# Performance work log

Hardware: AMD Instinct MI355X
Metric: run time of the kernel (lower is better)

## Reference

```python
import jax, jax.numpy as jnp
import numpy as np
import math

NUM_HEADS = 8


def setup_inputs() -> dict:
    key = jax.random.key(0)
    ks = jax.random.split(key, 6)
    b, s, e = 4, 2048, 512
    x = jax.random.normal(ks[0], (b, s, e), dtype=jnp.float32)
    # 0/1 adjacency matrix as float (it multiplies the scores in the module)
    adj = jax.random.randint(ks[1], (b, s, s), 0, 2).astype(jnp.float32)
    scale = 0.02
    Wqkv_w = jax.random.normal(ks[2], (3 * e, e), dtype=jnp.float32) * scale
    Wqkv_b = jax.random.normal(ks[3], (3 * e,), dtype=jnp.float32) * scale
    out_w = jax.random.normal(ks[4], (e, e), dtype=jnp.float32) * scale
    out_b = jax.random.normal(ks[5], (e,), dtype=jnp.float32) * scale
    return {"x": x, "adj": adj, "Wqkv_w": Wqkv_w, "Wqkv_b": Wqkv_b,
            "out_w": out_w, "out_b": out_b}


def reference(x, adj, Wqkv_w, Wqkv_b, out_w, out_b):
    b, s, e = x.shape
    h = NUM_HEADS
    d = e // h
    # fused qkv projection: (b, s, 3*e) -> (b, s, 3, h, d)
    qkv = (x @ Wqkv_w.T + Wqkv_b).reshape(b, s, 3, h, d)
    qkv = jnp.transpose(qkv, (2, 0, 3, 1, 4))  # (3, b, h, s, d)
    q, k, v = qkv[0], qkv[1], qkv[2]
    inv_sqrt_d = 1.0 / math.sqrt(d)
    scores = jnp.einsum('bhqd,bhkd->bhqk', q, k) * inv_sqrt_d
    scores = jnp.clip(scores * adj[:, None, :, :], -10000.0, 10000.0)
    attn = jax.nn.softmax(scores, axis=-1)
    out = jnp.einsum('bhqk,bhkd->bhqd', attn, v)
    out = jnp.transpose(out, (0, 2, 1, 3)).reshape(b, s, e)  # (b, s, h*d)
    return out @ out_w.T + out_b
```

## Files before the change

### kernel.cpp

```cpp
#include <hip/hip_runtime.h>


typedef __attribute__((ext_vector_type(8))) short bf16x8;
typedef __attribute__((ext_vector_type(4))) float f32x4;
typedef __attribute__((ext_vector_type(4))) unsigned short ushort4v;
typedef __attribute__((ext_vector_type(4))) _Float16 f16x4;
typedef __attribute__((ext_vector_type(2))) __fp16 h16x2;

#if __has_builtin(__builtin_amdgcn_exp2f)
#define EXP2F(x) __builtin_amdgcn_exp2f(x)
#else
#define EXP2F(x) exp2f(x)
#endif

#define QSCALE 0.18033688011112042f

__device__ __forceinline__ unsigned short f2bf(float f) {
  unsigned int u = __float_as_uint(f);
  u += 0x7FFFu + ((u >> 16) & 1u);
  return (unsigned short)(u >> 16);
}
__device__ __forceinline__ unsigned short f2h(float f) {
  union { _Float16 h; unsigned short u; } cv;
  cv.h = (_Float16)f;
  return cv.u;
}

__device__ __forceinline__ int sbit(unsigned w, int pos) {
  return ((int)(w << (31 - pos))) >> 31;
}

__device__ __forceinline__ f16x4 pk4(float p0, float p1, float p2, float p3) {
  union { struct { h16x2 a, b; } s; f16x4 v; } u;
  u.s.a = __builtin_amdgcn_cvt_pkrtz(p0, p1);
  u.s.b = __builtin_amdgcn_cvt_pkrtz(p2, p3);
  return u.v;
}

__global__ __launch_bounds__(256) void prep_k(const float* __restrict__ x,
                                              unsigned short* __restrict__ x_bf,
                                              const float* __restrict__ wqkv,
                                              unsigned short* __restrict__ wqkv_bf,
                                              const float* __restrict__ outw,
                                              unsigned short* __restrict__ outw_bf,
                                              const float* __restrict__ adj,
                                              unsigned long long* __restrict__ abits) {
  const int bid = blockIdx.x;
  if (bid < 5120) {
    const float* in; unsigned short* out; int i;
    if (bid < 4096) { in = x; out = x_bf; i = bid * 256 + threadIdx.x; }
    else if (bid < 4864) { in = wqkv; out = wqkv_bf; i = (bid - 4096) * 256 + threadIdx.x; }
    else { in = outw; out = outw_bf; i = (bid - 4864) * 256 + threadIdx.x; }
    float4 v = ((const float4*)in)[i];
    ushort4v o;
    o[0] = f2bf(v.x); o[1] = f2bf(v.y); o[2] = f2bf(v.z); o[3] = f2bf(v.w);
    ((ushort4v*)out)[i] = o;
  } else {
    const int gw = (bid - 5120) * 4 + (threadIdx.x >> 6);
    const int l = threadIdx.x & 63;
    const int b = gw >> 11, q = gw & 2047;
    const float* row = adj + ((size_t)b * 2048 + q) * 2048;
    unsigned long long* ob = abits + (size_t)b * 65536 + q;
#pragma unroll 4
    for (int kt = 0; kt < 32; ++kt) {
      const float v = row[kt * 64 + l];
      const unsigned long long m = __ballot(v != 0.f);
      if (l == 0) ob[(size_t)kt * 2048] = m;
    }
  }
}

template <int MODE>
__global__ __launch_bounds__(256, 3) void gemm128_k(const unsigned short* __restrict__ A,
                                                    const unsigned short* __restrict__ Bt,
                                                    const float* __restrict__ bias, int Kdim,
                                                    int Ntiles, unsigned short* __restrict__ q_out,
                                                    unsigned short* __restrict__ k_out,
                                                    unsigned short* __restrict__ v_out,
                                                    float* __restrict__ f_out) {
  __shared__ union {
    struct { unsigned short A[2][128][40], B[2][128][40]; } s;
    unsigned short T[64][136];
  } u;

  const int t = threadIdx.x;
  const int lane = t & 63, w = t >> 6, ln = lane & 15, quad = lane >> 4;
  const int mt = blockIdx.x / Ntiles, nt = blockIdx.x % Ntiles;
  const int wm = (w >> 1) * 64, wn = (w & 1) * 64;
  const int strow = t >> 2, stcol = (t & 3) * 8;

  const size_t abase = (size_t)(mt * 128 + strow) * Kdim + stcol;
  const size_t bbase = (size_t)(nt * 128 + strow) * Kdim + stcol;

  f32x4 acc[4][4];
#pragma unroll
  for (int i = 0; i < 4; ++i)
#pragma unroll
    for (int j = 0; j < 4; ++j) acc[i][j] = (f32x4){0.f, 0.f, 0.f, 0.f};

  bf16x8 a0 = *(const bf16x8*)(A + abase);
  bf16x8 a1 = *(const bf16x8*)(A + abase + (size_t)64 * Kdim);
  bf16x8 b0 = *(const bf16x8*)(Bt + bbase);
  bf16x8 b1 = *(const bf16x8*)(Bt + bbase + (size_t)64 * Kdim);
  *(bf16x8*)&u.s.A[0][strow][stcol] = a0;
  *(bf16x8*)&u.s.A[0][64 + strow][stcol] = a1;
  *(bf16x8*)&u.s.B[0][strow][stcol] = b0;
  *(bf16x8*)&u.s.B[0][64 + strow][stcol] = b1;
  __syncthreads();

  const int iters = Kdim >> 5;
  for (int it = 0; it < iters; ++it) {
    const int cur = it & 1, nxt = cur ^ 1;

    const int kn = ((it + 1) << 5) & (Kdim - 1);
    a0 = *(const bf16x8*)(A + abase + kn);
    a1 = *(const bf16x8*)(A + abase + (size_t)64 * Kdim + kn);
    b0 = *(const bf16x8*)(Bt + bbase + kn);
    b1 = *(const bf16x8*)(Bt + bbase + (size_t)64 * Kdim + kn);

    bf16x8 bfr[4];
#pragma unroll
    for (int nf = 0; nf < 4; ++nf)
      bfr[nf] = *(const bf16x8*)&u.s.B[cur][wn + nf * 16 + ln][quad * 8];
#pragma unroll
    for (int mf = 0; mf < 4; ++mf) {
      bf16x8 af = *(const bf16x8*)&u.s.A[cur][wm + mf * 16 + ln][quad * 8];
#pragma unroll
      for (int nf = 0; nf < 4; ++nf)
        acc[mf][nf] = __builtin_amdgcn_mfma_f32_16x16x32_bf16(af, bfr[nf], acc[mf][nf], 0, 0, 0);
    }

    if (it + 1 < iters) {
      *(bf16x8*)&u.s.A[nxt][strow][stcol] = a0;
      *(bf16x8*)&u.s.A[nxt][64 + strow][stcol] = a1;
      *(bf16x8*)&u.s.B[nxt][strow][stcol] = b0;
      *(bf16x8*)&u.s.B[nxt][64 + strow][stcol] = b1;
      __syncthreads();
    }
  }

  if (MODE == 0 && nt >= 8) {
    const int bb = mt >> 4, sq0 = (mt & 15) * 128;
#pragma unroll
    for (int half = 0; half < 2; ++half) {
      __syncthreads();
      if ((w & 1) == half) {
#pragma unroll
        for (int nf = 0; nf < 4; ++nf) {
          const float bv = bias[nt * 128 + half * 64 + nf * 16 + ln];
#pragma unroll
          for (int mf = 0; mf < 4; ++mf)
#pragma unroll
            for (int r = 0; r < 4; ++r)
              u.T[nf * 16 + ln][wm + mf * 16 + quad * 4 + r] = f2h(acc[mf][nf][r] + bv);
        }
      }
      __syncthreads();
#pragma unroll
      for (int rep = 0; rep < 4; ++rep) {
        const int row = rep * 16 + (t >> 4), c = t & 15;
        const bf16x8 val = *(const bf16x8*)&u.T[row][c * 8];
        const int hd = (nt - 8) * 128 + half * 64 + row;
        const int hh = hd >> 6, dd = hd & 63;
        *(bf16x8*)(v_out + ((size_t)(bb * 8 + hh) * 64 + dd) * 2048 + sq0 + c * 8) = val;
      }
    }
    return;
  }

#pragma unroll
  for (int mf = 0; mf < 4; ++mf) {
    const int m = mt * 128 + wm + mf * 16 + quad * 4;
#pragma unroll
    for (int nf = 0; nf < 4; ++nf) {
      const int n = nt * 128 + wn + nf * 16 + ln;
      const float bv = bias[n];
      if (MODE == 0) {
        const int hd = n & 511;
        const int hh = hd >> 6, dd = hd & 63;
        const int bb = m >> 11, sq = m & 2047;
        if (n < 512) {
#pragma unroll
          for (int r = 0; r < 4; ++r)
            q_out[((size_t)(bb * 8 + hh) * 2048 + sq + r) * 64 + dd] =
                f2bf((acc[mf][nf][r] + bv) * QSCALE);
        } else {
#pragma unroll
          for (int r = 0; r < 4; ++r)
            k_out[((size_t)(bb * 8 + hh) * 2048 + sq + r) * 64 + dd] = f2bf(acc[mf][nf][r] + bv);
        }
      } else {
#pragma unroll
        for (int r = 0; r < 4; ++r) f_out[(size_t)(m + r) * 512 + n] = acc[mf][nf][r] + bv;
      }
    }
  }
}

__global__ __launch_bounds__(256, 2) void attn_k(const unsigned short* __restrict__ Qg,
                                                 const unsigned short* __restrict__ Kg,
                                                 const unsigned short* __restrict__ Vg,
                                                 const unsigned long long* __restrict__ Mg,
                                                 unsigned short* __restrict__ Og) {
  __shared__ unsigned short K_lds[2][64][72];
  __shared__ unsigned short V_lds[2][64][72];
  __shared__ unsigned long long M_lds[2][128];

  const int t = threadIdx.x;
  const int w = t >> 6, lane = t & 63, ln = lane & 15, quad = lane >> 4;
  const int bh = blockIdx.x & 31, qt = blockIdx.x >> 5, bb = bh >> 3;
  const int sbase = qt * 128;

  const unsigned short* Qp = Qg + (size_t)bh * (2048 * 64);
  const unsigned short* Kp = Kg + (size_t)bh * (2048 * 64);
  const unsigned short* Vp = Vg + (size_t)bh * (64 * 2048);
  const unsigned long long* Mp = Mg + (size_t)bb * 65536 + sbase;

  bf16x8 qf[2][2];
#pragma unroll
  for (int qg = 0; qg < 2; ++qg) {
    const int qrow = sbase + w * 32 + qg * 16 + ln;
    qf[qg][0] = *(const bf16x8*)(Qp + (size_t)qrow * 64 + quad * 8);
    qf[qg][1] = *(const bf16x8*)(Qp + (size_t)qrow * 64 + 32 + quad * 8);
  }

  const _Float16 one_h = (_Float16)((ln == 0) ? 1.0f : 0.0f);
  const f16x4 vf_one = (f16x4){one_h, one_h, one_h, one_h};

  f32x4 acc_o[2][4];
#pragma unroll
  for (int qg = 0; qg < 2; ++qg)
#pragma unroll
    for (int dg = 0; dg < 4; ++dg) acc_o[qg][dg] = (f32x4){0.f, 0.f, 0.f, 0.f};
  f32x4 acc_1[2] = {(f32x4){0.f, 0.f, 0.f, 0.f}, (f32x4){0.f, 0.f, 0.f, 0.f}};

  const int strow = t >> 2;
  const int stcol = (t & 3) * 16;

  const unsigned short* Kl = Kp + (size_t)strow * 64 + stcol;
  const unsigned short* Vl = Vp + (size_t)strow * 2048 + stcol;

  bf16x8 kr0 = *(const bf16x8*)(Kl);
  bf16x8 kr1 = *(const bf16x8*)(Kl + 8);
  bf16x8 vr0 = *(const bf16x8*)(Vl);
  bf16x8 vr1 = *(const bf16x8*)(Vl + 8);
  unsigned long long mreg = (w < 2) ? Mp[w * 64 + lane] : 0ull;
  *(bf16x8*)&K_lds[0][strow][stcol] = kr0;
  *(bf16x8*)&K_lds[0][strow][stcol + 8] = kr1;
  *(bf16x8*)&V_lds[0][strow][stcol] = vr0;
  *(bf16x8*)&V_lds[0][strow][stcol + 8] = vr1;
  if (w < 2) M_lds[0][w * 64 + lane] = mreg;
  __syncthreads();

  const int mq = w * 32 + ln;
  const int qsh = quad * 4;

  for (int kt = 0; kt < 32; ++kt) {
    const int cur = kt & 1, nxt = cur ^ 1;

    kr0 = *(const bf16x8*)(Kl + (size_t)(kt + 1) * 4096);
    kr1 = *(const bf16x8*)(Kl + (size_t)(kt + 1) * 4096 + 8);
    vr0 = *(const bf16x8*)(Vl + (kt + 1) * 64);
    vr1 = *(const bf16x8*)(Vl + (kt + 1) * 64 + 8);
    mreg = (w < 2) ? Mp[(size_t)(kt + 1) * 2048 + w * 64 + lane] : 0ull;

    f32x4 sc[2][4];
#pragma unroll
    for (int nf = 0; nf < 4; ++nf) {
      bf16x8 kf0 = *(const bf16x8*)&K_lds[cur][nf * 16 + ln][quad * 8];
      bf16x8 kf1 = *(const bf16x8*)&K_lds[cur][nf * 16 + ln][32 + quad * 8];
#pragma unroll
      for (int qg = 0; qg < 2; ++qg) {
        f32x4 z = (f32x4){0.f, 0.f, 0.f, 0.f};
        z = __builtin_amdgcn_mfma_f32_16x16x32_bf16(kf0, qf[qg][0], z, 0, 0, 0);
        sc[qg][nf] = __builtin_amdgcn_mfma_f32_16x16x32_bf16(kf1, qf[qg][1], z, 0, 0, 0);
      }
    }

    f16x4 vfa[4][4];
#pragma unroll
    for (int ks = 0; ks < 4; ++ks)
#pragma unroll
      for (int dg = 0; dg < 4; ++dg)
        vfa[ks][dg] = *(const f16x4*)&V_lds[cur][dg * 16 + ln][ks * 16 + quad * 4];

    f16x4 pa[2][4];
#pragma unroll
    for (int qg = 0; qg < 2; ++qg) {
      const unsigned long long m64 = M_lds[cur][mq + qg * 16];
      const unsigned wlo = (unsigned)m64 >> qsh;
      const unsigned whi = (unsigned)(m64 >> 32) >> qsh;
#pragma unroll
      for (int nf = 0; nf < 4; ++nf) {
        const unsigned wm16 = ((nf & 2) ? whi : wlo) >> ((nf & 1) * 16);
        float p[4];
#pragma unroll
        for (int r = 0; r < 4; ++r) {
          const int se = sbit(wm16, r);
          const float s = __int_as_float(__float_as_int(sc[qg][nf][r]) & se);
          p[r] = EXP2F(s);
        }
        pa[qg][nf] = pk4(p[0], p[1], p[2], p[3]);
      }
    }

#pragma unroll
    for (int ks = 0; ks < 4; ++ks)
#pragma unroll
      for (int qg = 0; qg < 2; ++qg) {
#pragma unroll
        for (int dg = 0; dg < 4; ++dg)
          acc_o[qg][dg] =
              __builtin_amdgcn_mfma_f32_16x16x16f16(pa[qg][ks], vfa[ks][dg], acc_o[qg][dg], 0, 0, 0);
        acc_1[qg] = __builtin_amdgcn_mfma_f32_16x16x16f16(pa[qg][ks], vf_one, acc_1[qg], 0, 0, 0);
      }

    if (kt < 31) {
      *(bf16x8*)&K_lds[nxt][strow][stcol] = kr0;
      *(bf16x8*)&K_lds[nxt][strow][stcol + 8] = kr1;
      *(bf16x8*)&V_lds[nxt][strow][stcol] = vr0;
      *(bf16x8*)&V_lds[nxt][strow][stcol + 8] = vr1;
      if (w < 2) M_lds[nxt][w * 64 + lane] = mreg;
      __syncthreads();
    }
  }

  unsigned short* Op = Og + (size_t)bb * 2048 * 512 + (size_t)(bh & 7) * 64;
#pragma unroll
  for (int qg = 0; qg < 2; ++qg)
#pragma unroll
    for (int r = 0; r < 4; ++r) {
      const float inv = 1.0f / __shfl(acc_1[qg][r], quad * 16);
      const int sq = sbase + w * 32 + qg * 16 + quad * 4 + r;
#pragma unroll
      for (int dg = 0; dg < 4; ++dg)
        Op[(size_t)sq * 512 + dg * 16 + ln] = f2bf(acc_o[qg][dg][r] * inv);
    }
}

extern "C" void kernel_launch(void* const* d_in, const int* in_sizes, int n_in, void* d_out,
                              int out_size, void* d_ws, size_t ws_size, hipStream_t stream) {
  const float* x = (const float*)d_in[0];
  const float* adj = (const float*)d_in[1];
  const float* wqkv = (const float*)d_in[2];
  const float* bqkv = (const float*)d_in[3];
  const float* outw = (const float*)d_in[4];
  const float* outb = (const float*)d_in[5];
  float* out = (float*)d_out;

  char* ws = (char*)d_ws;
  unsigned short* x_bf = (unsigned short*)(ws);
  unsigned short* wqkv_bf = (unsigned short*)(ws + 8388608);
  unsigned short* outw_bf = (unsigned short*)(ws + 9961472);
  unsigned long long* abits = (unsigned long long*)(ws + 10485760);
  unsigned short* Qb = (unsigned short*)(ws + 27262976);
  unsigned short* Kb = (unsigned short*)(ws + 35651584);
  unsigned short* Vb = (unsigned short*)(ws + 44040192);
  unsigned short* Ob = (unsigned short*)(ws + 52428800);

  prep_k<<<7168, 256, 0, stream>>>(x, x_bf, wqkv, wqkv_bf, outw, outw_bf, adj, abits);

  gemm128_k<0><<<768, 256, 0, stream>>>(x_bf, wqkv_bf, bqkv, 512, 12, Qb, Kb, Vb, nullptr);

  attn_k<<<512, 256, 0, stream>>>(Qb, Kb, Vb, abits, Ob);

  gemm128_k<1><<<256, 256, 0, stream>>>(Ob, outw_bf, outb, 512, 4, nullptr, nullptr, nullptr, out);
}
```

Measured before the change: 220.1 us.

## Use 16x16x32 f16 MFMA for PV with permuted K rows, XCD-aware GEMM tiling

The attention kernel permutes which K rows each lane loads so the score fragments line up with the K-dimension layout of the wider 16x16x32 f16 MFMA. This halves the number of PV and row-sum MFMA instructions and lets V fragments be read as 8-wide vectors. The K LDS row padding changes from 72 to 76 to move bank conflicts caused by the new access pattern. The GEMM also remaps block indices so that consecutive M tiles are scheduled on the same XCD for better L2 reuse, which adds index arithmetic and relies on the grid size dividing evenly.

```diff
diff --git a/kernel.cpp b/kernel.cpp
--- a/kernel.cpp
+++ b/kernel.cpp
@@ -5,6 +5,7 @@
 typedef __attribute__((ext_vector_type(4))) float f32x4;
 typedef __attribute__((ext_vector_type(4))) unsigned short ushort4v;
 typedef __attribute__((ext_vector_type(4))) _Float16 f16x4;
+typedef __attribute__((ext_vector_type(8))) _Float16 f16x8;
 typedef __attribute__((ext_vector_type(2))) __fp16 h16x2;
 
 #if __has_builtin(__builtin_amdgcn_exp2f)
@@ -30,11 +31,24 @@
   return ((int)(w << (31 - pos))) >> 31;
 }
 
-__device__ __forceinline__ f16x4 pk4(float p0, float p1, float p2, float p3) {
-  union { struct { h16x2 a, b; } s; f16x4 v; } u;
-  u.s.a = __builtin_amdgcn_cvt_pkrtz(p0, p1);
-  u.s.b = __builtin_amdgcn_cvt_pkrtz(p2, p3);
+__device__ __forceinline__ f16x8 pk8(const float* p) {
+  union { struct { h16x2 a, b, c, d; } s; f16x8 v; } u;
+  u.s.a = __builtin_amdgcn_cvt_pkrtz(p[0], p[1]);
+  u.s.b = __builtin_amdgcn_cvt_pkrtz(p[2], p[3]);
+  u.s.c = __builtin_amdgcn_cvt_pkrtz(p[4], p[5]);
+  u.s.d = __builtin_amdgcn_cvt_pkrtz(p[6], p[7]);
   return u.v;
+}
+
+__device__ __forceinline__ f32x4 mfma_pv(f16x8 a, f16x8 b, f32x4 c) {
+#if __has_builtin(__builtin_amdgcn_mfma_f32_16x16x32_f16)
+  return __builtin_amdgcn_mfma_f32_16x16x32_f16(a, b, c, 0, 0, 0);
+#else
+  union { f16x8 v; struct { f16x4 lo, hi; } s; } ua, ub;
+  ua.v = a; ub.v = b;
+  c = __builtin_amdgcn_mfma_f32_16x16x16f16(ua.s.lo, ub.s.lo, c, 0, 0, 0);
+  return __builtin_amdgcn_mfma_f32_16x16x16f16(ua.s.hi, ub.s.hi, c, 0, 0, 0);
+#endif
 }
 
 __global__ __launch_bounds__(256) void prep_k(const float* __restrict__ x,
@@ -85,7 +99,9 @@
 
   const int t = threadIdx.x;
   const int lane = t & 63, w = t >> 6, ln = lane & 15, quad = lane >> 4;
-  const int mt = blockIdx.x / Ntiles, nt = blockIdx.x % Ntiles;
+  const int xcd = blockIdx.x & 7, loc = blockIdx.x >> 3;
+  const int mt = xcd * ((gridDim.x >> 3) / Ntiles) + loc / Ntiles;
+  const int nt = loc % Ntiles;
   const int wm = (w >> 1) * 64, wn = (w & 1) * 64;
   const int strow = t >> 2, stcol = (t & 3) * 8;
 
@@ -202,7 +218,7 @@
                                                  const unsigned short* __restrict__ Vg,
                                                  const unsigned long long* __restrict__ Mg,
                                                  unsigned short* __restrict__ Og) {
-  __shared__ unsigned short K_lds[2][64][72];
+  __shared__ unsigned short K_lds[2][64][76];
   __shared__ unsigned short V_lds[2][64][72];
   __shared__ unsigned long long M_lds[2][128];
 
@@ -225,7 +241,7 @@
   }
 
   const _Float16 one_h = (_Float16)((ln == 0) ? 1.0f : 0.0f);
-  const f16x4 vf_one = (f16x4){one_h, one_h, one_h, one_h};
+  const f16x8 vf_one = (f16x8){one_h, one_h, one_h, one_h, one_h, one_h, one_h, one_h};
 
   f32x4 acc_o[2][4];
 #pragma unroll
@@ -253,7 +269,7 @@
   __syncthreads();
 
   const int mq = w * 32 + ln;
-  const int qsh = quad * 4;
+  const int kperm = ((ln >> 2) << 3) + (ln & 3);
 
   for (int kt = 0; kt < 32; ++kt) {
     const int cur = kt & 1, nxt = cur ^ 1;
@@ -266,53 +282,56 @@
 
     f32x4 sc[2][4];
 #pragma unroll
-    for (int nf = 0; nf < 4; ++nf) {
-      bf16x8 kf0 = *(const bf16x8*)&K_lds[cur][nf * 16 + ln][quad * 8];
-      bf16x8 kf1 = *(const bf16x8*)&K_lds[cur][nf * 16 + ln][32 + quad * 8];
-#pragma unroll
-      for (int qg = 0; qg < 2; ++qg) {
-        f32x4 z = (f32x4){0.f, 0.f, 0.f, 0.f};
-        z = __builtin_amdgcn_mfma_f32_16x16x32_bf16(kf0, qf[qg][0], z, 0, 0, 0);
-        sc[qg][nf] = __builtin_amdgcn_mfma_f32_16x16x32_bf16(kf1, qf[qg][1], z, 0, 0, 0);
-      }
-    }
-
-    f16x4 vfa[4][4];
-#pragma unroll
-    for (int ks = 0; ks < 4; ++ks)
+    for (int h = 0; h < 2; ++h)
+#pragma unroll
+      for (int e = 0; e < 2; ++e) {
+        const int krow = h * 32 + kperm + e * 4;
+        bf16x8 kf0 = *(const bf16x8*)&K_lds[cur][krow][quad * 8];
+        bf16x8 kf1 = *(const bf16x8*)&K_lds[cur][krow][32 + quad * 8];
+#pragma unroll
+        for (int qg = 0; qg < 2; ++qg) {
+          f32x4 z = (f32x4){0.f, 0.f, 0.f, 0.f};
+          z = __builtin_amdgcn_mfma_f32_16x16x32_bf16(kf0, qf[qg][0], z, 0, 0, 0);
+          sc[qg][h * 2 + e] = __builtin_amdgcn_mfma_f32_16x16x32_bf16(kf1, qf[qg][1], z, 0, 0, 0);
+        }
+      }
+
+    f16x8 vfa[2][4];
+#pragma unroll
+    for (int h = 0; h < 2; ++h)
 #pragma unroll
       for (int dg = 0; dg < 4; ++dg)
-        vfa[ks][dg] = *(const f16x4*)&V_lds[cur][dg * 16 + ln][ks * 16 + quad * 4];
-
-    f16x4 pa[2][4];
+        vfa[h][dg] = *(const f16x8*)&V_lds[cur][dg * 16 + ln][h * 32 + quad * 8];
+
+    f16x8 pa[2][2];
 #pragma unroll
     for (int qg = 0; qg < 2; ++qg) {
       const unsigned long long m64 = M_lds[cur][mq + qg * 16];
-      const unsigned wlo = (unsigned)m64 >> qsh;
-      const unsigned whi = (unsigned)(m64 >> 32) >> qsh;
-#pragma unroll
-      for (int nf = 0; nf < 4; ++nf) {
-        const unsigned wm16 = ((nf & 2) ? whi : wlo) >> ((nf & 1) * 16);
-        float p[4];
-#pragma unroll
-        for (int r = 0; r < 4; ++r) {
-          const int se = sbit(wm16, r);
-          const float s = __int_as_float(__float_as_int(sc[qg][nf][r]) & se);
-          p[r] = EXP2F(s);
-        }
-        pa[qg][nf] = pk4(p[0], p[1], p[2], p[3]);
-      }
-    }
-
-#pragma unroll
-    for (int ks = 0; ks < 4; ++ks)
+#pragma unroll
+      for (int h = 0; h < 2; ++h) {
+        const unsigned wrd = (h ? (unsigned)(m64 >> 32) : (unsigned)m64) >> (quad * 8);
+        float p[8];
+#pragma unroll
+        for (int e = 0; e < 2; ++e)
+#pragma unroll
+          for (int r = 0; r < 4; ++r) {
+            const int j = e * 4 + r;
+            const int se = sbit(wrd, j);
+            const float s = __int_as_float(__float_as_int(sc[qg][h * 2 + e][r]) & se);
+            p[j] = EXP2F(s);
+          }
+        pa[qg][h] = pk8(p);
+      }
+    }
+
+#pragma unroll
+    for (int h = 0; h < 2; ++h)
 #pragma unroll
       for (int qg = 0; qg < 2; ++qg) {
 #pragma unroll
         for (int dg = 0; dg < 4; ++dg)
-          acc_o[qg][dg] =
-              __builtin_amdgcn_mfma_f32_16x16x16f16(pa[qg][ks], vfa[ks][dg], acc_o[qg][dg], 0, 0, 0);
-        acc_1[qg] = __builtin_amdgcn_mfma_f32_16x16x16f16(pa[qg][ks], vf_one, acc_1[qg], 0, 0, 0);
+          acc_o[qg][dg] = mfma_pv(pa[qg][h], vfa[h][dg], acc_o[qg][dg]);
+        acc_1[qg] = mfma_pv(pa[qg][h], vf_one, acc_1[qg]);
       }
 
     if (kt < 31) {
```

Result: faster. 215.7 us (-2.0%).
